# Kernel optimization log

Hardware: AMD Instinct MI355X
Metric: run time of the kernel (lower is better)

Reference implementation:

```python
import jax, jax.numpy as jnp
import numpy as np

BRANCH = 8
LEVELS = 7
N = (BRANCH ** LEVELS - 1) // (BRANCH - 1)  # 299593 nodes, complete 8-ary tree
VOCAB, IN_DIM, MEM = 50000, 300, 150


def _tree_structure():
    parent = np.empty(N, np.int32)
    parent[0] = N  # sentinel: root scatters into dropped segment N
    idx = np.arange(1, N)
    parent[1:] = (idx - 1) // BRANCH
    depth = np.empty(N, np.int32)
    start = 0
    for d in range(LEVELS):
        cnt = BRANCH ** d
        depth[start:start + cnt] = d
        start += cnt
    return jnp.asarray(parent), jnp.asarray(depth)


def setup_inputs() -> dict:
    key = jax.random.key(0)
    ks = jax.random.split(key, 20)
    parent, depth = _tree_structure()
    inp = {
        'tokens': jax.random.randint(ks[0], (N,), 0, VOCAB, dtype=jnp.int32),
        'parent': parent,
        'depth': depth,
        'max_depth': LEVELS,
        'emb': jax.random.normal(ks[1], (VOCAB, IN_DIM), jnp.float32) * 0.1,
    }
    names_x = ['Wix', 'Wfx', 'Wox', 'Wux']
    names_h = ['Wih', 'Wfh', 'Woh', 'Wuh']
    sx = 1.0 / np.sqrt(IN_DIM)
    sh = 1.0 / np.sqrt(MEM)
    for j, (nx, nh) in enumerate(zip(names_x, names_h)):
        inp[nx] = jax.random.normal(ks[2 + 4 * j], (MEM, IN_DIM), jnp.float32) * sx
        inp['b' + nx[1:]] = jax.random.normal(ks[3 + 4 * j], (MEM,), jnp.float32) * sx
        inp[nh] = jax.random.normal(ks[4 + 4 * j], (MEM, MEM), jnp.float32) * sh
        inp['b' + nh[1:]] = jax.random.normal(ks[5 + 4 * j], (MEM,), jnp.float32) * sh
    return inp


def reference(tokens, parent, depth, max_depth, emb,
              Wix, bix, Wih, bih, Wfx, bfx, Wfh, bfh,
              Wox, box, Woh, boh, Wux, bux, Wuh, buh):
    n = tokens.shape[0]
    x = emb[tokens]  # [N, in_dim]
    # precompute all input-side gate projections once (batched GEMMs)
    ix_x = x @ Wix.T + bix
    fx_x = x @ Wfx.T + bfx
    ox_x = x @ Wox.T + box
    ux_x = x @ Wux.T + bux
    # parent index safe for gathering (root's sentinel -> 0; its row is masked out)
    gparent = jnp.where(parent >= n, 0, parent)

    h = jnp.zeros((n, MEM), x.dtype)
    c = jnp.zeros((n, MEM), x.dtype)

    # level-synchronous bottom-up sweep (loop over tree depth, not data)
    for d in range(max_depth - 1, -1, -1):
        # per-child forget gate: sigmoid(fh(h_child) + fx(x_parent)) * c_child
        f = jax.nn.sigmoid(h @ Wfh.T + bfh + fx_x[gparent])
        fc_sum = jax.ops.segment_sum(f * c, parent, num_segments=n + 1)[:n]
        h_sum = jax.ops.segment_sum(h, parent, num_segments=n + 1)[:n]
        i = jax.nn.sigmoid(ix_x + h_sum @ Wih.T + bih)
        o = jax.nn.sigmoid(ox_x + h_sum @ Woh.T + boh)
        u = jnp.tanh(ux_x + h_sum @ Wuh.T + buh)
        c_new = i * u + fc_sum
        h_new = o * jnp.tanh(c_new)
        mask = (depth == d)[:, None]
        c = jnp.where(mask, c_new, c)
        h = jnp.where(mask, h_new, h)
    # original returns concatenated cell states (post-order); here indexed by node id
    return c
```

## Files before the change

kernel.cpp:

```cpp
#include <hip/hip_runtime.h>


#define MEMD  150
#define IND   300
#define NINT  37449
#define VOCAB 50000
#define GROW  600
#define FSTR  152

typedef short bf16x8 __attribute__((ext_vector_type(8)));
typedef float f32x16 __attribute__((ext_vector_type(16)));
#define ZERO16 {0,0,0,0,0,0,0,0,0,0,0,0,0,0,0,0}

#define GALL_OFF 0ul
#define FHX_OFF  60000000ul
#define HSB_OFF  67600000ul
#define FCS_OFF  79000000ul
#define BPX_OFF  90400000ul
#define BPH_OFF  90800000ul

__device__ __forceinline__ float b2f(unsigned short u) {
    union { unsigned int i; float f; } v; v.i = ((unsigned int)u) << 16; return v.f;
}
__device__ __forceinline__ unsigned short f2b(float f) {
    union { float f; unsigned int i; } v; v.f = f;
    unsigned int x = v.i;
    x += 0x7fffu + ((x >> 16) & 1u);
    return (unsigned short)(x >> 16);
}
__device__ __forceinline__ float sigm(float x) {
    return __builtin_amdgcn_rcpf(1.0f + __expf(-x));
}
__device__ __forceinline__ float tanh_fast(float x) {
    float e = __expf(2.0f * x);
    return 1.0f - 2.0f * __builtin_amdgcn_rcpf(e + 1.0f);
}
__device__ __forceinline__ unsigned char f2e4m3(float f) {
    union { float f; unsigned u; } v; v.f = f;
    unsigned s = (v.u >> 31) << 7;
    float af = fabsf(f);
    if (af >= 448.f) return (unsigned char)(s | 0x7E);
    if (af < 0.015625f) {
        int m = (int)(af * 512.f + 0.5f);
        if (m > 7) m = 7;
        return (unsigned char)(s | m);
    }
    unsigned u = v.u & 0x7fffffffu;
    u += 0x7ffffu + ((u >> 20) & 1u);
    int ef = (int)(u >> 23) - 120;
    unsigned m = (u >> 20) & 7u;
    if (ef < 1) { ef = 1; m = 0; }
    if (ef > 15) { ef = 15; m = 6; }
    return (unsigned char)(s | (ef << 3) | m);
}
__device__ __forceinline__ float e4m3f(unsigned char u) {
    unsigned s = (u >> 7) & 1u, ef = (u >> 3) & 15u, m = u & 7u;
    if (ef == 0) {
        float r = (float)m * 0.001953125f;
        return s ? -r : r;
    }
    union { unsigned u; float f; } v;
    v.u = (s << 31) | ((ef + 120) << 23) | (m << 20);
    return v.f;
}

__global__ void pack_w(const float* __restrict__ Wix, const float* __restrict__ Wox,
                       const float* __restrict__ Wux, const float* __restrict__ Wfx,
                       const float* __restrict__ Wih, const float* __restrict__ Woh,
                       const float* __restrict__ Wuh, const float* __restrict__ Wfh,
                       unsigned short* __restrict__ bpx, unsigned short* __restrict__ bph)
{
    const int total_x = 4 * 5 * 19 * 512;
    const int total_h = 4 * 5 * 10 * 512;
    for (int i = blockIdx.x * blockDim.x + threadIdx.x; i < total_x + total_h;
         i += gridDim.x * blockDim.x) {
        if (i < total_x) {
            int e = i & 7, lane = (i >> 3) & 63, rest = i >> 9;
            int ks = rest % 19; rest /= 19;
            int nt = rest % 5;  int g = rest / 5;
            int col = nt * 32 + (lane & 31);
            int k = ks * 16 + ((lane >> 5) << 3) + e;
            const float* W = (g == 0) ? Wix : (g == 1) ? Wox : (g == 2) ? Wux : Wfx;
            bpx[i] = f2b((col < MEMD && k < IND) ? W[col * IND + k] : 0.f);
        } else {
            int j = i - total_x;
            int e = j & 7, lane = (j >> 3) & 63, rest = j >> 9;
            int ks = rest % 10; rest /= 10;
            int nt = rest % 5;  int g = rest / 5;
            int col = nt * 32 + (lane & 31);
            int k = ks * 16 + ((lane >> 5) << 3) + e;
            const float* W = (g == 0) ? Wih : (g == 1) ? Woh : (g == 2) ? Wuh : Wfh;
            bph[j] = f2b((col < MEMD && k < MEMD) ? W[col * MEMD + k] : 0.f);
        }
    }
}

__global__ __launch_bounds__(640, 2)
void vocab_gemm(const float* __restrict__ emb,
                const float* __restrict__ bix, const float* __restrict__ bih,
                const float* __restrict__ box_, const float* __restrict__ boh,
                const float* __restrict__ bux, const float* __restrict__ buh,
                const float* __restrict__ bfx, const float* __restrict__ bfh,
                const unsigned short* __restrict__ bpx_u,
                unsigned short* __restrict__ gall)
{
    __shared__ __align__(16) char sm0[40960];
    const int tid = threadIdx.x, lane = tid & 63, w = tid >> 6;
    const int hi = lane >> 5, ln31 = lane & 31;
    const int tile0 = blockIdx.x * 64;
    const int rowsValid = min(64, VOCAB - tile0);
    const int mt = (w >= 5) ? 1 : 0, nt = w - mt * 5;

    for (int i = tid; i < 64 * 40; i += 640) {
        int r = i / 40, q = i % 40;
        int rr = (r < rowsValid) ? r : 0;
        const float* er = emb + (long)(tile0 + rr) * IND;
        float4 v0 = {0.f,0.f,0.f,0.f}, v1 = {0.f,0.f,0.f,0.f};
        if (q < 38) v0 = *(const float4*)(er + q * 8);
        if (q < 37) v1 = *(const float4*)(er + q * 8 + 4);
        bf16x8 p;
        p[0]=(short)f2b(v0.x); p[1]=(short)f2b(v0.y); p[2]=(short)f2b(v0.z); p[3]=(short)f2b(v0.w);
        p[4]=(short)f2b(v1.x); p[5]=(short)f2b(v1.y); p[6]=(short)f2b(v1.z); p[7]=(short)f2b(v1.w);
        *(bf16x8*)(sm0 + r * 640 + ((q * 16) ^ ((r & 7) << 4))) = p;
    }
    __syncthreads();

    const bf16x8* BX = (const bf16x8*)bpx_u;
    const int row = mt * 32 + ln31;
    const int col = nt * 32 + ln31;
    const bool colv = col < MEMD;
    const int cc = colv ? col : 0;
    const float* b1[4] = {bix, box_, bux, bfx};
    const float* b2[4] = {bih, boh, buh, bfh};

    for (int g = 0; g < 4; ++g) {
        f32x16 acc = ZERO16;
        bf16x8 aC = *(const bf16x8*)(sm0 + row * 640 + ((hi * 16) ^ ((row & 7) << 4)));
        bf16x8 bC = BX[((g * 5 + nt) * 19 + 0) * 64 + lane];
        #pragma unroll
        for (int ks = 0; ks < 19; ++ks) {
            bf16x8 aN, bN;
            if (ks < 18) {
                aN = *(const bf16x8*)(sm0 + row * 640 + (((ks + 1) * 32 + hi * 16) ^ ((row & 7) << 4)));
                bN = BX[((g * 5 + nt) * 19 + ks + 1) * 64 + lane];
            }
            acc = __builtin_amdgcn_mfma_f32_32x32x16_bf16(aC, bC, acc, 0, 0, 0);
            aC = aN; bC = bN;
        }
        float bias = colv ? (b1[g][cc] + b2[g][cc]) : 0.f;
        #pragma unroll
        for (int r = 0; r < 16; ++r) {
            int rloc = mt * 32 + (r & 3) + 8 * (r >> 2) + 4 * hi;
            if (rloc < rowsValid && colv)
                gall[(long)(tile0 + rloc) * GROW + col * 4 + g] = f2b(acc[r] + bias);
        }
    }
}

__global__ __launch_bounds__(256, 8)
void hleaf_k(const unsigned short* __restrict__ gall, unsigned short* __restrict__ htmp)
{
    int i = blockIdx.x * 256 + threadIdx.x;
    if (i >= VOCAB * FSTR) return;
    int v = i / FSTR, col = i % FSTR;
    unsigned short r = 0;
    if (col < MEMD) {
        ushort4 gv = *(const ushort4*)(gall + (long)v * GROW + col * 4);
        float iv = sigm(b2f(gv.x));
        float ov = sigm(b2f(gv.y));
        float uv = tanh_fast(b2f(gv.z));
        float cv = iv * uv;
        r = f2b(ov * tanh_fast(cv));
    }
    htmp[i] = r;
}

__global__ __launch_bounds__(320, 4)
void fhx_gemm(const unsigned short* __restrict__ htmp,
              const unsigned short* __restrict__ bph_u,
              unsigned char* __restrict__ fhx)
{
    __shared__ __align__(16) char sm0[12288];
    const int tid = threadIdx.x, lane = tid & 63, w = tid >> 6;
    const int hi = lane >> 5, ln31 = lane & 31;
    const int tile0 = blockIdx.x * 32;
    const int rowsValid = min(32, VOCAB - tile0);
    const int nt = w;

    for (int i = tid; i < 32 * 20; i += 320) {
        int r = i / 20, q = i % 20;
        int rr = (r < rowsValid) ? r : 0;
        bf16x8 v = {0,0,0,0,0,0,0,0};
        if (q < 19) v = *(const bf16x8*)(htmp + (long)(tile0 + rr) * FSTR + q * 8);
        *(bf16x8*)(sm0 + r * 384 + ((q * 16) ^ ((r & 7) << 4))) = v;
    }
    __syncthreads();

    const bf16x8* BH = (const bf16x8*)bph_u;
    const int row = ln31;
    f32x16 ff = ZERO16;
    #pragma unroll
    for (int ks = 0; ks < 10; ++ks) {
        bf16x8 a = *(const bf16x8*)(sm0 + row * 384 + ((ks * 32 + hi * 16) ^ ((row & 7) << 4)));
        ff = __builtin_amdgcn_mfma_f32_32x32x16_bf16(a, BH[((15 + nt) * 10 + ks) * 64 + lane], ff, 0, 0, 0);
    }
    const int col = nt * 32 + ln31;
    if (col < MEMD) {
        #pragma unroll
        for (int r = 0; r < 16; ++r) {
            int rloc = (r & 3) + 8 * (r >> 2) + 4 * hi;
            if (rloc < rowsValid)
                fhx[(long)(tile0 + rloc) * FSTR + col] = f2e4m3(ff[r]);
        }
    }
}

__global__ __launch_bounds__(320, 8)
void leaf_csum(const int* __restrict__ tokens,
               const unsigned short* __restrict__ gall,
               const unsigned char* __restrict__ fhx,
               unsigned short* __restrict__ hsumb, unsigned short* __restrict__ fcs,
               float* __restrict__ c_out)
{
    __shared__ int ctok[16];
    __shared__ int ptokL[2];
    const int tid = threadIdx.x;
    const int pl = tid / 160;
    const int col0 = tid % 160;
    const bool colv = col0 < MEMD;
    const int col = colv ? col0 : (MEMD - 1);
    const int pidx = blockIdx.x * 2 + pl;
    const int pnode = 4681 + pidx;
    const long cbase = 8L * pnode + 1;
    if (tid < 16) ctok[tid] = tokens[37449 + blockIdx.x * 16 + tid];
    if (tid < 2)  ptokL[tid] = tokens[4681 + blockIdx.x * 2 + tid];
    __syncthreads();

    const float fxp = b2f(gall[(long)ptokL[pl] * GROW + col * 4 + 3]);
    float hs = 0.f, fc = 0.f;
    #pragma unroll
    for (int k = 0; k < 8; ++k) {
        int ct = ctok[pl * 8 + k];
        ushort4 gv = *(const ushort4*)(gall + (long)ct * GROW + col * 4);
        float iv = sigm(b2f(gv.x));
        float ov = sigm(b2f(gv.y));
        float uv = tanh_fast(b2f(gv.z));
        float cv = iv * uv;
        float h = ov * tanh_fast(cv);
        float f = sigm(e4m3f(fhx[(long)ct * FSTR + col]) + fxp);
        hs += h;
        fc += f * cv;
        if (colv) c_out[(cbase + k) * MEMD + col] = cv;
    }
    if (colv) {
        hsumb[(long)pnode * FSTR + col] = f2b(hs);
        fcs[(long)pnode * FSTR + col]  = f2b(fc);
    }
}

__global__ __launch_bounds__(320, 2)
void level_k(const int* __restrict__ tokens,
             const unsigned short* __restrict__ gall,
             const unsigned short* __restrict__ bph_u,
             unsigned short* __restrict__ hsumb, unsigned short* __restrict__ fcsum,
             float* __restrict__ c_out, int base, int cnt, int writePar)
{
    __shared__ __align__(16) char sm0[24576];
    __shared__ int toksL[32];
    __shared__ int ptokL[4];
    const int tid = threadIdx.x, lane = tid & 63, w = tid >> 6;
    const int hi = lane >> 5, ln31 = lane & 31;
    const int tile0 = blockIdx.x * 32;
    const int nodeBase = base + tile0;
    const int rowsValid = min(32, cnt - tile0);
    const int p0 = (nodeBase - 1) >> 3;
    const int nt = w;

    if (tid < 32) toksL[tid] = tokens[nodeBase + ((tid < rowsValid) ? tid : 0)];
    if (writePar && tid < 4) ptokL[tid] = tokens[p0 + tid];
    for (int i = tid; i < 32 * 20; i += 320) {
        int r = i / 20, q = i % 20;
        int rr = (r < rowsValid) ? r : 0;
        bf16x8 v = {0,0,0,0,0,0,0,0};
        if (q < 19)
            v = *(const bf16x8*)(hsumb + (long)(nodeBase + rr) * FSTR + q * 8);
        *(bf16x8*)(sm0 + 12288 + r * 384 + ((q * 16) ^ ((r & 7) << 4))) = v;
    }
    __syncthreads();

    const bf16x8* BH = (const bf16x8*)bph_u;
    const int row = ln31;
    const int col = nt * 32 + ln31;
    const bool colv = col < MEMD;
    const int cc = colv ? col : 0;

    f32x16 ai = ZERO16, ao = ZERO16, au = ZERO16;
    {
        const char* hb = sm0 + 12288;
        bf16x8 aC = *(const bf16x8*)(hb + row * 384 + ((hi * 16) ^ ((row & 7) << 4)));
        bf16x8 b0C = BH[((0 * 5 + nt) * 10 + 0) * 64 + lane];
        bf16x8 b1C = BH[((1 * 5 + nt) * 10 + 0) * 64 + lane];
        bf16x8 b2C = BH[((2 * 5 + nt) * 10 + 0) * 64 + lane];
        #pragma unroll
        for (int ks = 0; ks < 10; ++ks) {
            bf16x8 aN, b0N, b1N, b2N;
            if (ks < 9) {
                aN  = *(const bf16x8*)(hb + row * 384 + (((ks + 1) * 32 + hi * 16) ^ ((row & 7) << 4)));
                b0N = BH[((0 * 5 + nt) * 10 + ks + 1) * 64 + lane];
                b1N = BH[((1 * 5 + nt) * 10 + ks + 1) * 64 + lane];
                b2N = BH[((2 * 5 + nt) * 10 + ks + 1) * 64 + lane];
            }
            ai = __builtin_amdgcn_mfma_f32_32x32x16_bf16(aC, b0C, ai, 0, 0, 0);
            ao = __builtin_amdgcn_mfma_f32_32x32x16_bf16(aC, b1C, ao, 0, 0, 0);
            au = __builtin_amdgcn_mfma_f32_32x32x16_bf16(aC, b2C, au, 0, 0, 0);
            aC = aN; b0C = b0N; b1C = b1N; b2C = b2N;
        }
    }

    float cvv[16];
    {
        float hp[4] = {0.f, 0.f, 0.f, 0.f};
        #pragma unroll
        for (int r = 0; r < 16; ++r) {
            int rloc = (r & 3) + 8 * (r >> 2) + 4 * hi;
            bool rv = rloc < rowsValid;
            ushort4 gv = *(const ushort4*)(gall + (long)toksL[rloc] * GROW + cc * 4);
            float fcin = (rv && colv) ? b2f(fcsum[(long)(nodeBase + rloc) * FSTR + col]) : 0.f;
            float iv = sigm(ai[r] + b2f(gv.x));
            float ov = sigm(ao[r] + b2f(gv.y));
            float uv = tanh_fast(au[r] + b2f(gv.z));
            float cv = iv * uv + fcin;
            float h = (rv && colv) ? ov * tanh_fast(cv) : 0.f;
            cvv[r] = (rv && colv) ? cv : 0.f;
            if (rv && colv) c_out[(long)(nodeBase + rloc) * MEMD + col] = cv;
            *(unsigned short*)(sm0 + rloc * 384 + ((col * 2) ^ ((rloc & 7) << 4))) = f2b(h);
            hp[r >> 2] += h;
        }
        if (writePar) {
            #pragma unroll
            for (int o = 0; o < 4; ++o) {
                float s = hp[o] + __shfl_xor(hp[o], 32);
                if (lane < 32 && colv && o * 8 < rowsValid)
                    hsumb[(long)(p0 + o) * FSTR + col] = f2b(s);
            }
        }
    }
    __syncthreads();

    if (writePar) {
        f32x16 ff = ZERO16;
        {
            bf16x8 aC = *(const bf16x8*)(sm0 + row * 384 + ((hi * 16) ^ ((row & 7) << 4)));
            bf16x8 bC = BH[((15 + nt) * 10 + 0) * 64 + lane];
            #pragma unroll
            for (int ks = 0; ks < 10; ++ks) {
                bf16x8 aN, bN;
                if (ks < 9) {
                    aN = *(const bf16x8*)(sm0 + row * 384 + (((ks + 1) * 32 + hi * 16) ^ ((row & 7) << 4)));
                    bN = BH[((15 + nt) * 10 + ks + 1) * 64 + lane];
                }
                ff = __builtin_amdgcn_mfma_f32_32x32x16_bf16(aC, bC, ff, 0, 0, 0);
                aC = aN; bC = bN;
            }
        }
        #pragma unroll
        for (int o = 0; o < 4; ++o) {
            float fx = b2f(gall[(long)ptokL[o] * GROW + cc * 4 + 3]);
            float fp = 0.f;
            #pragma unroll
            for (int q = 0; q < 4; ++q) {
                int r = o * 4 + q;
                fp += sigm(ff[r] + fx) * cvv[r];
            }
            float s = fp + __shfl_xor(fp, 32);
            if (lane < 32 && colv && o * 8 < rowsValid)
                fcsum[(long)(p0 + o) * FSTR + col] = f2b(s);
        }
    }
}

__global__ __launch_bounds__(320, 2)
void tail_k(const int* __restrict__ tokens,
            const unsigned short* __restrict__ gall,
            const unsigned short* __restrict__ bph_u,
            unsigned short* __restrict__ hsumb, unsigned short* __restrict__ fcsum,
            float* __restrict__ c_out)
{
    __shared__ __align__(16) char sm0[24576];
    __shared__ int toksL[32];
    __shared__ int ptokL[4];
    const int tid = threadIdx.x, lane = tid & 63, w = tid >> 6;
    const int hi = lane >> 5, ln31 = lane & 31;
    const int nt = w;
    const bf16x8* BH = (const bf16x8*)bph_u;
    const int row = ln31;
    const int col = nt * 32 + ln31;
    const bool colv = col < MEMD;
    const int cc = colv ? col : 0;

    const int basesL[3] = {9, 1, 0};
    const int cntsL[3]  = {64, 8, 1};
    const int wpL[3]    = {1, 1, 0};

    for (int li = 0; li < 3; ++li) {
        for (int t0 = 0; t0 < cntsL[li]; t0 += 32) {
            const int nodeBase = basesL[li] + t0;
            const int rowsValid = min(32, cntsL[li] - t0);
            const int p0 = (nodeBase - 1) >> 3;
            const int writePar = wpL[li];

            if (tid < 32) toksL[tid] = tokens[nodeBase + ((tid < rowsValid) ? tid : 0)];
            if (writePar && tid < 4) ptokL[tid] = tokens[p0 + tid];
            for (int i = tid; i < 32 * 20; i += 320) {
                int r = i / 20, q = i % 20;
                int rr = (r < rowsValid) ? r : 0;
                bf16x8 v = {0,0,0,0,0,0,0,0};
                if (q < 19)
                    v = *(const bf16x8*)(hsumb + (long)(nodeBase + rr) * FSTR + q * 8);
                *(bf16x8*)(sm0 + 12288 + r * 384 + ((q * 16) ^ ((r & 7) << 4))) = v;
            }
            __syncthreads();

            f32x16 ai = ZERO16, ao = ZERO16, au = ZERO16;
            {
                const char* hb = sm0 + 12288;
                #pragma unroll
                for (int ks = 0; ks < 10; ++ks) {
                    bf16x8 a = *(const bf16x8*)(hb + row * 384 + ((ks * 32 + hi * 16) ^ ((row & 7) << 4)));
                    ai = __builtin_amdgcn_mfma_f32_32x32x16_bf16(a, BH[((0 * 5 + nt) * 10 + ks) * 64 + lane], ai, 0, 0, 0);
                    ao = __builtin_amdgcn_mfma_f32_32x32x16_bf16(a, BH[((1 * 5 + nt) * 10 + ks) * 64 + lane], ao, 0, 0, 0);
                    au = __builtin_amdgcn_mfma_f32_32x32x16_bf16(a, BH[((2 * 5 + nt) * 10 + ks) * 64 + lane], au, 0, 0, 0);
                }
            }

            float cvv[16];
            {
                float hp[4] = {0.f, 0.f, 0.f, 0.f};
                #pragma unroll
                for (int r = 0; r < 16; ++r) {
                    int rloc = (r & 3) + 8 * (r >> 2) + 4 * hi;
                    bool rv = rloc < rowsValid;
                    ushort4 gv = *(const ushort4*)(gall + (long)toksL[rloc] * GROW + cc * 4);
                    float fcin = (rv && colv) ? b2f(fcsum[(long)(nodeBase + rloc) * FSTR + col]) : 0.f;
                    float iv = sigm(ai[r] + b2f(gv.x));
                    float ov = sigm(ao[r] + b2f(gv.y));
                    float uv = tanh_fast(au[r] + b2f(gv.z));
                    float cv = iv * uv + fcin;
                    float h = (rv && colv) ? ov * tanh_fast(cv) : 0.f;
                    cvv[r] = (rv && colv) ? cv : 0.f;
                    if (rv && colv) c_out[(long)(nodeBase + rloc) * MEMD + col] = cv;
                    *(unsigned short*)(sm0 + rloc * 384 + ((col * 2) ^ ((rloc & 7) << 4))) = f2b(h);
                    hp[r >> 2] += h;
                }
                if (writePar) {
                    #pragma unroll
                    for (int o = 0; o < 4; ++o) {
                        float s = hp[o] + __shfl_xor(hp[o], 32);
                        if (lane < 32 && colv && o * 8 < rowsValid)
                            hsumb[(long)(p0 + o) * FSTR + col] = f2b(s);
                    }
                }
            }
            __syncthreads();

            if (writePar) {
                f32x16 ff = ZERO16;
                #pragma unroll
                for (int ks = 0; ks < 10; ++ks) {
                    bf16x8 a = *(const bf16x8*)(sm0 + row * 384 + ((ks * 32 + hi * 16) ^ ((row & 7) << 4)));
                    ff = __builtin_amdgcn_mfma_f32_32x32x16_bf16(a, BH[((15 + nt) * 10 + ks) * 64 + lane], ff, 0, 0, 0);
                }
                #pragma unroll
                for (int o = 0; o < 4; ++o) {
                    float fx = b2f(gall[(long)ptokL[o] * GROW + cc * 4 + 3]);
                    float fp = 0.f;
                    #pragma unroll
                    for (int q = 0; q < 4; ++q)
                        fp += sigm(ff[o * 4 + q] + fx) * cvv[o * 4 + q];
                    float s = fp + __shfl_xor(fp, 32);
                    if (lane < 32 && colv && o * 8 < rowsValid)
                        fcsum[(long)(p0 + o) * FSTR + col] = f2b(s);
                }
            }
            __syncthreads();
        }
    }
}

extern "C" void kernel_launch(void* const* d_in, const int* in_sizes, int n_in,
                              void* d_out, int out_size, void* d_ws, size_t ws_size,
                              hipStream_t stream) {
    const int*   tokens = (const int*)d_in[0];
    const float* emb = (const float*)d_in[4];
    const float* Wix = (const float*)d_in[5];  const float* bix = (const float*)d_in[6];
    const float* Wih = (const float*)d_in[7];  const float* bih = (const float*)d_in[8];
    const float* Wfx = (const float*)d_in[9];  const float* bfx = (const float*)d_in[10];
    const float* Wfh = (const float*)d_in[11]; const float* bfh = (const float*)d_in[12];
    const float* Wox = (const float*)d_in[13]; const float* box_ = (const float*)d_in[14];
    const float* Woh = (const float*)d_in[15]; const float* boh = (const float*)d_in[16];
    const float* Wux = (const float*)d_in[17]; const float* bux = (const float*)d_in[18];
    const float* Wuh = (const float*)d_in[19]; const float* buh = (const float*)d_in[20];
    float* c_out = (float*)d_out;
    char* ws = (char*)d_ws;

    unsigned short* gall  = (unsigned short*)(ws + GALL_OFF);
    unsigned char*  fhx   = (unsigned char*)(ws + FHX_OFF);
    unsigned short* hsumb = (unsigned short*)(ws + HSB_OFF);
    unsigned short* htmp  = (unsigned short*)(ws + HSB_OFF);
    unsigned short* fcs   = (unsigned short*)(ws + FCS_OFF);
    unsigned short* bpx   = (unsigned short*)(ws + BPX_OFF);
    unsigned short* bph   = (unsigned short*)(ws + BPH_OFF);

    pack_w<<<128, 512, 0, stream>>>(Wix, Wox, Wux, Wfx, Wih, Woh, Wuh, Wfh, bpx, bph);
    vocab_gemm<<<(VOCAB + 63) / 64, 640, 0, stream>>>(
        emb, bix, bih, box_, boh, bux, buh, bfx, bfh, bpx, gall);
    hleaf_k<<<(VOCAB * FSTR + 255) / 256, 256, 0, stream>>>(gall, htmp);
    fhx_gemm<<<(VOCAB + 31) / 32, 320, 0, stream>>>(htmp, bph, fhx);
    leaf_csum<<<16384, 320, 0, stream>>>(tokens, gall, fhx, hsumb, fcs, c_out);

    static const int bases[7] = {0, 1, 9, 73, 585, 4681, 37449};
    static const int cnts[7]  = {1, 8, 64, 512, 4096, 32768, 262144};
    for (int d = 5; d >= 3; --d) {
        int grid = (cnts[d] + 31) / 32;
        level_k<<<grid, 320, 0, stream>>>(
            tokens, gall, bph, hsumb, fcs, c_out, bases[d], cnts[d], 1);
    }
    tail_k<<<1, 320, 0, stream>>>(tokens, gall, bph, hsumb, fcs, c_out);
}
```

Measured before the change: 332.7 us.

## Fuse leaf gate activations into vocab GEMM and precompute per-node internal gates

The vocabulary GEMM now computes only the i/o/u gates and immediately applies the leaf activations. It writes the leaf cell and hidden states in bf16 and drops the separate hleaf_k pass and the 4-gate interleaved gall table. A new xint_gemm computes all four input projections per internal node in node order. Level, tail and leaf kernels can then read gate inputs contiguously instead of through a token-indexed gather. The leaf cell-state scratch lives in the output buffer, which is safe only because later writes land past that region. The change adds a second GEMM over internal nodes in exchange for less elementwise recomputation and less scattered memory traffic in leaf_csum.

```diff
diff --git a/kernel.cpp b/kernel.cpp
--- a/kernel.cpp
+++ b/kernel.cpp
@@ -5,19 +5,20 @@
 #define IND   300
 #define NINT  37449
 #define VOCAB 50000
-#define GROW  600
+#define XROW  608
 #define FSTR  152
 
 typedef short bf16x8 __attribute__((ext_vector_type(8)));
 typedef float f32x16 __attribute__((ext_vector_type(16)));
 #define ZERO16 {0,0,0,0,0,0,0,0,0,0,0,0,0,0,0,0}
 
-#define GALL_OFF 0ul
-#define FHX_OFF  60000000ul
-#define HSB_OFF  67600000ul
-#define FCS_OFF  79000000ul
-#define BPX_OFF  90400000ul
-#define BPH_OFF  90800000ul
+#define XINT_OFF 0ul
+#define HLF_OFF  45540000ul
+#define FHX_OFF  60740000ul
+#define HSB_OFF  68340000ul
+#define FCS_OFF  79730000ul
+#define BPX_OFF  91120000ul
+#define BPH_OFF  91510000ul
 
 __device__ __forceinline__ float b2f(unsigned short u) {
     union { unsigned int i; float f; } v; v.i = ((unsigned int)u) << 16; return v.f;
@@ -95,23 +96,21 @@
     }
 }
 
-__global__ __launch_bounds__(640, 2)
-void vocab_gemm(const float* __restrict__ emb,
+__global__ __launch_bounds__(320, 2)
+void cleaf_gemm(const float* __restrict__ emb,
                 const float* __restrict__ bix, const float* __restrict__ bih,
                 const float* __restrict__ box_, const float* __restrict__ boh,
                 const float* __restrict__ bux, const float* __restrict__ buh,
-                const float* __restrict__ bfx, const float* __restrict__ bfh,
                 const unsigned short* __restrict__ bpx_u,
-                unsigned short* __restrict__ gall)
-{
-    __shared__ __align__(16) char sm0[40960];
+                unsigned short* __restrict__ cleafU, unsigned short* __restrict__ hleaf)
+{
+    __shared__ __align__(16) char sm0[20480];
     const int tid = threadIdx.x, lane = tid & 63, w = tid >> 6;
     const int hi = lane >> 5, ln31 = lane & 31;
-    const int tile0 = blockIdx.x * 64;
-    const int rowsValid = min(64, VOCAB - tile0);
-    const int mt = (w >= 5) ? 1 : 0, nt = w - mt * 5;
-
-    for (int i = tid; i < 64 * 40; i += 640) {
+    const int tile0 = blockIdx.x * 32;
+    const int rowsValid = min(32, VOCAB - tile0);
+
+    for (int i = tid; i < 32 * 40; i += 320) {
         int r = i / 40, q = i % 40;
         int rr = (r < rowsValid) ? r : 0;
         const float* er = emb + (long)(tile0 + rr) * IND;
@@ -126,57 +125,132 @@
     __syncthreads();
 
     const bf16x8* BX = (const bf16x8*)bpx_u;
-    const int row = mt * 32 + ln31;
+    const int row = ln31, nt = w;
     const int col = nt * 32 + ln31;
     const bool colv = col < MEMD;
     const int cc = colv ? col : 0;
-    const float* b1[4] = {bix, box_, bux, bfx};
-    const float* b2[4] = {bih, boh, buh, bfh};
-
-    for (int g = 0; g < 4; ++g) {
-        f32x16 acc = ZERO16;
+
+    f32x16 a0 = ZERO16, a1 = ZERO16, a2 = ZERO16;
+    {
         bf16x8 aC = *(const bf16x8*)(sm0 + row * 640 + ((hi * 16) ^ ((row & 7) << 4)));
-        bf16x8 bC = BX[((g * 5 + nt) * 19 + 0) * 64 + lane];
+        bf16x8 b0C = BX[((0 * 5 + nt) * 19 + 0) * 64 + lane];
+        bf16x8 b1C = BX[((1 * 5 + nt) * 19 + 0) * 64 + lane];
+        bf16x8 b2C = BX[((2 * 5 + nt) * 19 + 0) * 64 + lane];
         #pragma unroll
         for (int ks = 0; ks < 19; ++ks) {
-            bf16x8 aN, bN;
+            bf16x8 aN, b0N, b1N, b2N;
             if (ks < 18) {
-                aN = *(const bf16x8*)(sm0 + row * 640 + (((ks + 1) * 32 + hi * 16) ^ ((row & 7) << 4)));
-                bN = BX[((g * 5 + nt) * 19 + ks + 1) * 64 + lane];
-            }
-            acc = __builtin_amdgcn_mfma_f32_32x32x16_bf16(aC, bC, acc, 0, 0, 0);
-            aC = aN; bC = bN;
-        }
-        float bias = colv ? (b1[g][cc] + b2[g][cc]) : 0.f;
+                aN  = *(const bf16x8*)(sm0 + row * 640 + (((ks + 1) * 32 + hi * 16) ^ ((row & 7) << 4)));
+                b0N = BX[((0 * 5 + nt) * 19 + ks + 1) * 64 + lane];
+                b1N = BX[((1 * 5 + nt) * 19 + ks + 1) * 64 + lane];
+                b2N = BX[((2 * 5 + nt) * 19 + ks + 1) * 64 + lane];
+            }
+            a0 = __builtin_amdgcn_mfma_f32_32x32x16_bf16(aC, b0C, a0, 0, 0, 0);
+            a1 = __builtin_amdgcn_mfma_f32_32x32x16_bf16(aC, b1C, a1, 0, 0, 0);
+            a2 = __builtin_amdgcn_mfma_f32_32x32x16_bf16(aC, b2C, a2, 0, 0, 0);
+            aC = aN; b0C = b0N; b1C = b1N; b2C = b2N;
+        }
+    }
+    const float bi = bix[cc] + bih[cc];
+    const float bo = box_[cc] + boh[cc];
+    const float bu = bux[cc] + buh[cc];
+    #pragma unroll
+    for (int r = 0; r < 16; ++r) {
+        int rloc = (r & 3) + 8 * (r >> 2) + 4 * hi;
+        float iv = sigm(a0[r] + bi);
+        float ov = sigm(a1[r] + bo);
+        float uv = tanh_fast(a2[r] + bu);
+        float cv = iv * uv;
+        float h = ov * tanh_fast(cv);
+        if (rloc < rowsValid && colv) {
+            long o = (long)(tile0 + rloc) * FSTR + col;
+            cleafU[o] = f2b(cv);
+            hleaf[o] = f2b(h);
+        }
+    }
+}
+
+__global__ __launch_bounds__(320, 2)
+void xint_gemm(const int* __restrict__ tokens, const float* __restrict__ emb,
+               const float* __restrict__ bix, const float* __restrict__ bih,
+               const float* __restrict__ box_, const float* __restrict__ boh,
+               const float* __restrict__ bux, const float* __restrict__ buh,
+               const float* __restrict__ bfx, const float* __restrict__ bfh,
+               const unsigned short* __restrict__ bpx_u,
+               unsigned short* __restrict__ xint)
+{
+    __shared__ __align__(16) char sm0[20480];
+    __shared__ int toksL[32];
+    const int tid = threadIdx.x, lane = tid & 63, w = tid >> 6;
+    const int hi = lane >> 5, ln31 = lane & 31;
+    const int tile0 = blockIdx.x * 32;
+    const int rowsValid = min(32, NINT - tile0);
+
+    if (tid < 32) toksL[tid] = tokens[tile0 + ((tid < rowsValid) ? tid : 0)];
+    __syncthreads();
+    for (int i = tid; i < 32 * 40; i += 320) {
+        int r = i / 40, q = i % 40;
+        const float* er = emb + (long)toksL[r] * IND;
+        float4 v0 = {0.f,0.f,0.f,0.f}, v1 = {0.f,0.f,0.f,0.f};
+        if (q < 38) v0 = *(const float4*)(er + q * 8);
+        if (q < 37) v1 = *(const float4*)(er + q * 8 + 4);
+        bf16x8 p;
+        p[0]=(short)f2b(v0.x); p[1]=(short)f2b(v0.y); p[2]=(short)f2b(v0.z); p[3]=(short)f2b(v0.w);
+        p[4]=(short)f2b(v1.x); p[5]=(short)f2b(v1.y); p[6]=(short)f2b(v1.z); p[7]=(short)f2b(v1.w);
+        *(bf16x8*)(sm0 + r * 640 + ((q * 16) ^ ((r & 7) << 4))) = p;
+    }
+    __syncthreads();
+
+    const bf16x8* BX = (const bf16x8*)bpx_u;
+    const int row = ln31, nt = w;
+    const int col = nt * 32 + ln31;
+    const bool colv = col < MEMD;
+    const int cc = colv ? col : 0;
+
+    f32x16 a0 = ZERO16, a1 = ZERO16, a2 = ZERO16, a3 = ZERO16;
+    {
+        bf16x8 aC = *(const bf16x8*)(sm0 + row * 640 + ((hi * 16) ^ ((row & 7) << 4)));
+        bf16x8 b0C = BX[((0 * 5 + nt) * 19 + 0) * 64 + lane];
+        bf16x8 b1C = BX[((1 * 5 + nt) * 19 + 0) * 64 + lane];
+        bf16x8 b2C = BX[((2 * 5 + nt) * 19 + 0) * 64 + lane];
+        bf16x8 b3C = BX[((3 * 5 + nt) * 19 + 0) * 64 + lane];
         #pragma unroll
-        for (int r = 0; r < 16; ++r) {
-            int rloc = mt * 32 + (r & 3) + 8 * (r >> 2) + 4 * hi;
-            if (rloc < rowsValid && colv)
-                gall[(long)(tile0 + rloc) * GROW + col * 4 + g] = f2b(acc[r] + bias);
-        }
-    }
-}
-
-__global__ __launch_bounds__(256, 8)
-void hleaf_k(const unsigned short* __restrict__ gall, unsigned short* __restrict__ htmp)
-{
-    int i = blockIdx.x * 256 + threadIdx.x;
-    if (i >= VOCAB * FSTR) return;
-    int v = i / FSTR, col = i % FSTR;
-    unsigned short r = 0;
-    if (col < MEMD) {
-        ushort4 gv = *(const ushort4*)(gall + (long)v * GROW + col * 4);
-        float iv = sigm(b2f(gv.x));
-        float ov = sigm(b2f(gv.y));
-        float uv = tanh_fast(b2f(gv.z));
-        float cv = iv * uv;
-        r = f2b(ov * tanh_fast(cv));
-    }
-    htmp[i] = r;
+        for (int ks = 0; ks < 19; ++ks) {
+            bf16x8 aN, b0N, b1N, b2N, b3N;
+            if (ks < 18) {
+                aN  = *(const bf16x8*)(sm0 + row * 640 + (((ks + 1) * 32 + hi * 16) ^ ((row & 7) << 4)));
+                b0N = BX[((0 * 5 + nt) * 19 + ks + 1) * 64 + lane];
+                b1N = BX[((1 * 5 + nt) * 19 + ks + 1) * 64 + lane];
+                b2N = BX[((2 * 5 + nt) * 19 + ks + 1) * 64 + lane];
+                b3N = BX[((3 * 5 + nt) * 19 + ks + 1) * 64 + lane];
+            }
+            a0 = __builtin_amdgcn_mfma_f32_32x32x16_bf16(aC, b0C, a0, 0, 0, 0);
+            a1 = __builtin_amdgcn_mfma_f32_32x32x16_bf16(aC, b1C, a1, 0, 0, 0);
+            a2 = __builtin_amdgcn_mfma_f32_32x32x16_bf16(aC, b2C, a2, 0, 0, 0);
+            a3 = __builtin_amdgcn_mfma_f32_32x32x16_bf16(aC, b3C, a3, 0, 0, 0);
+            aC = aN; b0C = b0N; b1C = b1N; b2C = b2N; b3C = b3N;
+        }
+    }
+    const float bi = bix[cc] + bih[cc];
+    const float bo = box_[cc] + boh[cc];
+    const float bu = bux[cc] + buh[cc];
+    const float bf = bfx[cc] + bfh[cc];
+    #pragma unroll
+    for (int r = 0; r < 16; ++r) {
+        int rloc = (r & 3) + 8 * (r >> 2) + 4 * hi;
+        if (rloc < rowsValid && colv) {
+            ushort4 gv;
+            gv.x = f2b(a0[r] + bi);
+            gv.y = f2b(a1[r] + bo);
+            gv.z = f2b(a2[r] + bu);
+            gv.w = f2b(a3[r] + bf);
+            *(ushort4*)(xint + (long)(tile0 + rloc) * XROW + col * 4) = gv;
+        }
+    }
 }
 
 __global__ __launch_bounds__(320, 4)
-void fhx_gemm(const unsigned short* __restrict__ htmp,
+void fhx_gemm(const unsigned short* __restrict__ hleaf,
               const unsigned short* __restrict__ bph_u,
               unsigned char* __restrict__ fhx)
 {
@@ -191,7 +265,7 @@
         int r = i / 20, q = i % 20;
         int rr = (r < rowsValid) ? r : 0;
         bf16x8 v = {0,0,0,0,0,0,0,0};
-        if (q < 19) v = *(const bf16x8*)(htmp + (long)(tile0 + rr) * FSTR + q * 8);
+        if (q < 19) v = *(const bf16x8*)(hleaf + (long)(tile0 + rr) * FSTR + q * 8);
         *(bf16x8*)(sm0 + r * 384 + ((q * 16) ^ ((r & 7) << 4))) = v;
     }
     __syncthreads();
@@ -217,37 +291,33 @@
 
 __global__ __launch_bounds__(320, 8)
 void leaf_csum(const int* __restrict__ tokens,
-               const unsigned short* __restrict__ gall,
+               const unsigned short* __restrict__ cleafU,
+               const unsigned short* __restrict__ hleaf,
                const unsigned char* __restrict__ fhx,
+               const unsigned short* __restrict__ xint,
                unsigned short* __restrict__ hsumb, unsigned short* __restrict__ fcs,
                float* __restrict__ c_out)
 {
     __shared__ int ctok[16];
-    __shared__ int ptokL[2];
     const int tid = threadIdx.x;
     const int pl = tid / 160;
     const int col0 = tid % 160;
     const bool colv = col0 < MEMD;
     const int col = colv ? col0 : (MEMD - 1);
-    const int pidx = blockIdx.x * 2 + pl;
-    const int pnode = 4681 + pidx;
+    const int pnode = 4681 + blockIdx.x * 2 + pl;
     const long cbase = 8L * pnode + 1;
     if (tid < 16) ctok[tid] = tokens[37449 + blockIdx.x * 16 + tid];
-    if (tid < 2)  ptokL[tid] = tokens[4681 + blockIdx.x * 2 + tid];
-    __syncthreads();
-
-    const float fxp = b2f(gall[(long)ptokL[pl] * GROW + col * 4 + 3]);
+    __syncthreads();
+
+    const float fxp = b2f(xint[(long)pnode * XROW + col * 4 + 3]);
     float hs = 0.f, fc = 0.f;
     #pragma unroll
     for (int k = 0; k < 8; ++k) {
         int ct = ctok[pl * 8 + k];
-        ushort4 gv = *(const ushort4*)(gall + (long)ct * GROW + col * 4);
-        float iv = sigm(b2f(gv.x));
-        float ov = sigm(b2f(gv.y));
-        float uv = tanh_fast(b2f(gv.z));
-        float cv = iv * uv;
-        float h = ov * tanh_fast(cv);
-        float f = sigm(e4m3f(fhx[(long)ct * FSTR + col]) + fxp);
+        long o = (long)ct * FSTR + col;
+        float cv = b2f(cleafU[o]);
+        float h  = b2f(hleaf[o]);
+        float f  = sigm(e4m3f(fhx[o]) + fxp);
         hs += h;
         fc += f * cv;
         if (colv) c_out[(cbase + k) * MEMD + col] = cv;
@@ -259,15 +329,12 @@
 }
 
 __global__ __launch_bounds__(320, 2)
-void level_k(const int* __restrict__ tokens,
-             const unsigned short* __restrict__ gall,
+void level_k(const unsigned short* __restrict__ xint,
              const unsigned short* __restrict__ bph_u,
              unsigned short* __restrict__ hsumb, unsigned short* __restrict__ fcsum,
              float* __restrict__ c_out, int base, int cnt, int writePar)
 {
     __shared__ __align__(16) char sm0[24576];
-    __shared__ int toksL[32];
-    __shared__ int ptokL[4];
     const int tid = threadIdx.x, lane = tid & 63, w = tid >> 6;
     const int hi = lane >> 5, ln31 = lane & 31;
     const int tile0 = blockIdx.x * 32;
@@ -276,8 +343,6 @@
     const int p0 = (nodeBase - 1) >> 3;
     const int nt = w;
 
-    if (tid < 32) toksL[tid] = tokens[nodeBase + ((tid < rowsValid) ? tid : 0)];
-    if (writePar && tid < 4) ptokL[tid] = tokens[p0 + tid];
     for (int i = tid; i < 32 * 20; i += 320) {
         int r = i / 20, q = i % 20;
         int rr = (r < rowsValid) ? r : 0;
@@ -324,7 +389,8 @@
         for (int r = 0; r < 16; ++r) {
             int rloc = (r & 3) + 8 * (r >> 2) + 4 * hi;
             bool rv = rloc < rowsValid;
-            ushort4 gv = *(const ushort4*)(gall + (long)toksL[rloc] * GROW + cc * 4);
+            int rr = rv ? rloc : 0;
+            ushort4 gv = *(const ushort4*)(xint + (long)(nodeBase + rr) * XROW + cc * 4);
             float fcin = (rv && colv) ? b2f(fcsum[(long)(nodeBase + rloc) * FSTR + col]) : 0.f;
             float iv = sigm(ai[r] + b2f(gv.x));
             float ov = sigm(ao[r] + b2f(gv.y));
@@ -365,7 +431,7 @@
         }
         #pragma unroll
         for (int o = 0; o < 4; ++o) {
-            float fx = b2f(gall[(long)ptokL[o] * GROW + cc * 4 + 3]);
+            float fx = b2f(xint[(long)(p0 + o) * XROW + cc * 4 + 3]);
             float fp = 0.f;
             #pragma unroll
             for (int q = 0; q < 4; ++q) {
@@ -380,15 +446,12 @@
 }
 
 __global__ __launch_bounds__(320, 2)
-void tail_k(const int* __restrict__ tokens,
-            const unsigned short* __restrict__ gall,
+void tail_k(const unsigned short* __restrict__ xint,
             const unsigned short* __restrict__ bph_u,
             unsigned short* __restrict__ hsumb, unsigned short* __restrict__ fcsum,
             float* __restrict__ c_out)
 {
     __shared__ __align__(16) char sm0[24576];
-    __shared__ int toksL[32];
-    __shared__ int ptokL[4];
     const int tid = threadIdx.x, lane = tid & 63, w = tid >> 6;
     const int hi = lane >> 5, ln31 = lane & 31;
     const int nt = w;
@@ -403,20 +466,21 @@
     const int wpL[3]    = {1, 1, 0};
 
     for (int li = 0; li < 3; ++li) {
+        const int nodeBase = basesL[li];
+        const int rowsValid = min(32, cntsL[li]);
+        const int p0 = (nodeBase - 1) >> 3;
+        const int writePar = wpL[li];
         for (int t0 = 0; t0 < cntsL[li]; t0 += 32) {
-            const int nodeBase = basesL[li] + t0;
-            const int rowsValid = min(32, cntsL[li] - t0);
-            const int p0 = (nodeBase - 1) >> 3;
-            const int writePar = wpL[li];
-
-            if (tid < 32) toksL[tid] = tokens[nodeBase + ((tid < rowsValid) ? tid : 0)];
-            if (writePar && tid < 4) ptokL[tid] = tokens[p0 + tid];
+            const int nb = nodeBase + t0;
+            const int rv32 = min(32, cntsL[li] - t0);
+            const int pp0 = (nb - 1) >> 3;
+
             for (int i = tid; i < 32 * 20; i += 320) {
                 int r = i / 20, q = i % 20;
-                int rr = (r < rowsValid) ? r : 0;
+                int rr = (r < rv32) ? r : 0;
                 bf16x8 v = {0,0,0,0,0,0,0,0};
                 if (q < 19)
-                    v = *(const bf16x8*)(hsumb + (long)(nodeBase + rr) * FSTR + q * 8);
+                    v = *(const bf16x8*)(hsumb + (long)(nb + rr) * FSTR + q * 8);
                 *(bf16x8*)(sm0 + 12288 + r * 384 + ((q * 16) ^ ((r & 7) << 4))) = v;
             }
             __syncthreads();
@@ -439,16 +503,17 @@
                 #pragma unroll
                 for (int r = 0; r < 16; ++r) {
                     int rloc = (r & 3) + 8 * (r >> 2) + 4 * hi;
-                    bool rv = rloc < rowsValid;
-                    ushort4 gv = *(const ushort4*)(gall + (long)toksL[rloc] * GROW + cc * 4);
-                    float fcin = (rv && colv) ? b2f(fcsum[(long)(nodeBase + rloc) * FSTR + col]) : 0.f;
+                    bool rv = rloc < rv32;
+                    int rr = rv ? rloc : 0;
+                    ushort4 gv = *(const ushort4*)(xint + (long)(nb + rr) * XROW + cc * 4);
+                    float fcin = (rv && colv) ? b2f(fcsum[(long)(nb + rloc) * FSTR + col]) : 0.f;
                     float iv = sigm(ai[r] + b2f(gv.x));
                     float ov = sigm(ao[r] + b2f(gv.y));
                     float uv = tanh_fast(au[r] + b2f(gv.z));
                     float cv = iv * uv + fcin;
                     float h = (rv && colv) ? ov * tanh_fast(cv) : 0.f;
                     cvv[r] = (rv && colv) ? cv : 0.f;
-                    if (rv && colv) c_out[(long)(nodeBase + rloc) * MEMD + col] = cv;
+                    if (rv && colv) c_out[(long)(nb + rloc) * MEMD + col] = cv;
                     *(unsigned short*)(sm0 + rloc * 384 + ((col * 2) ^ ((rloc & 7) << 4))) = f2b(h);
                     hp[r >> 2] += h;
                 }
@@ -456,8 +521,8 @@
                     #pragma unroll
                     for (int o = 0; o < 4; ++o) {
                         float s = hp[o] + __shfl_xor(hp[o], 32);
-                        if (lane < 32 && colv && o * 8 < rowsValid)
-                            hsumb[(long)(p0 + o) * FSTR + col] = f2b(s);
+                        if (lane < 32 && colv && o * 8 < rv32)
+                            hsumb[(long)(pp0 + o) * FSTR + col] = f2b(s);
                     }
                 }
             }
@@ -472,14 +537,14 @@
                 }
                 #pragma unroll
                 for (int o = 0; o < 4; ++o) {
-                    float fx = b2f(gall[(long)ptokL[o] * GROW + cc * 4 + 3]);
+                    float fx = b2f(xint[(long)(pp0 + o) * XROW + cc * 4 + 3]);
                     float fp = 0.f;
                     #pragma unroll
                     for (int q = 0; q < 4; ++q)
                         fp += sigm(ff[o * 4 + q] + fx) * cvv[o * 4 + q];
                     float s = fp + __shfl_xor(fp, 32);
-                    if (lane < 32 && colv && o * 8 < rowsValid)
-                        fcsum[(long)(p0 + o) * FSTR + col] = f2b(s);
+                    if (lane < 32 && colv && o * 8 < rv32)
+                        fcsum[(long)(pp0 + o) * FSTR + col] = f2b(s);
                 }
             }
             __syncthreads();
@@ -503,27 +568,29 @@
     float* c_out = (float*)d_out;
     char* ws = (char*)d_ws;
 
-    unsigned short* gall  = (unsigned short*)(ws + GALL_OFF);
+    unsigned short* xint  = (unsigned short*)(ws + XINT_OFF);
+    unsigned short* hleaf = (unsigned short*)(ws + HLF_OFF);
     unsigned char*  fhx   = (unsigned char*)(ws + FHX_OFF);
     unsigned short* hsumb = (unsigned short*)(ws + HSB_OFF);
-    unsigned short* htmp  = (unsigned short*)(ws + HSB_OFF);
     unsigned short* fcs   = (unsigned short*)(ws + FCS_OFF);
     unsigned short* bpx   = (unsigned short*)(ws + BPX_OFF);
     unsigned short* bph   = (unsigned short*)(ws + BPH_OFF);
+    unsigned short* cleafU = (unsigned short*)d_out;
 
     pack_w<<<128, 512, 0, stream>>>(Wix, Wox, Wux, Wfx, Wih, Woh, Wuh, Wfh, bpx, bph);
-    vocab_gemm<<<(VOCAB + 63) / 64, 640, 0, stream>>>(
-        emb, bix, bih, box_, boh, bux, buh, bfx, bfh, bpx, gall);
-    hleaf_k<<<(VOCAB * FSTR + 255) / 256, 256, 0, stream>>>(gall, htmp);
-    fhx_gemm<<<(VOCAB + 31) / 32, 320, 0, stream>>>(htmp, bph, fhx);
-    leaf_csum<<<16384, 320, 0, stream>>>(tokens, gall, fhx, hsumb, fcs, c_out);
-
-    static const int bases[7] = {0, 1, 9, 73, 585, 4681, 37449};
-    static const int cnts[7]  = {1, 8, 64, 512, 4096, 32768, 262144};
-    for (int d = 5; d >= 3; --d) {
+    cleaf_gemm<<<(VOCAB + 31) / 32, 320, 0, stream>>>(
+        emb, bix, bih, box_, boh, bux, buh, bpx, cleafU, hleaf);
+    xint_gemm<<<(NINT + 31) / 32, 320, 0, stream>>>(
+        tokens, emb, bix, bih, box_, boh, bux, buh, bfx, bfh, bpx, xint);
+    fhx_gemm<<<(VOCAB + 31) / 32, 320, 0, stream>>>(hleaf, bph, fhx);
+    leaf_csum<<<16384, 320, 0, stream>>>(tokens, cleafU, hleaf, fhx, xint, hsumb, fcs, c_out);
+
+    static const int bases[3] = {4681, 585, 73};
+    static const int cnts[3]  = {32768, 4096, 512};
+    for (int d = 0; d < 3; ++d) {
         int grid = (cnts[d] + 31) / 32;
         level_k<<<grid, 320, 0, stream>>>(
-            tokens, gall, bph, hsumb, fcs, c_out, bases[d], cnts[d], 1);
-    }
-    tail_k<<<1, 320, 0, stream>>>(tokens, gall, bph, hsumb, fcs, c_out);
-}
+            xint, bph, hsumb, fcs, c_out, bases[d], cnts[d], 1);
+    }
+    tail_k<<<1, 320, 0, stream>>>(xint, bph, hsumb, fcs, c_out);
+}
```

Measured after the change: 278.8 us. 16.2% less time.
